# Kernel tuning notes

Hardware: AMD Instinct MI355X
Metric: run time of the kernel (lower is better)

The kernel has to match this reference:

```python
import jax, jax.numpy as jnp
import numpy as np

THRESH = 1.0   # kwargs_spikes['thresh']
VRESET = 0.0   # kwargs_spikes['vreset'] (not None -> hard reset branch)

@jax.custom_vjp
def rectangle_spike(x):
    # Rectangle surrogate-gradient spike fn: forward heaviside
    return (x >= 0.0).astype(x.dtype)

def _rs_fwd(x):
    return rectangle_spike(x), x

def _rs_bwd(x, g):
    # rectangular surrogate: grad passes where |u - thresh| < 0.5
    return (g * (jnp.abs(x) < 0.5).astype(g.dtype),)

rectangle_spike.defvjp(_rs_fwd, _rs_bwd)

def conv2d(x, w, b):
    # NCHW same-padding conv (padding = kernel_size // 2 with k=3 == SAME)
    y = jax.lax.conv_general_dilated(x, w, (1, 1), 'SAME',
                                     dimension_numbers=('NCHW', 'OIHW', 'NCHW'))
    return y + b[None, :, None, None]

def setup_inputs() -> dict:
    key = jax.random.key(0)
    ks = jax.random.split(key, 4)
    B, T, Cin, H, W = 8, 5, 64, 64, 64
    Cout, K = 64, 3
    # event-frame style sparse binary input
    events = (jax.random.uniform(ks[0], (B, T, Cin, H, W)) < 0.3).astype(jnp.float32)
    scale_in = 1.0 / np.sqrt(Cin * K * K)
    w_in = (jax.random.normal(ks[1], (2 * Cout, Cin, K, K)) * scale_in).astype(jnp.float32)
    b_in = jnp.zeros((2 * Cout,), jnp.float32)
    scale_g = 1.0 / np.sqrt(Cout * K * K)
    w_gate = (jax.random.normal(ks[2], (2 * Cout, Cout, K, K)) * scale_g).astype(jnp.float32)
    b_gate = jnp.zeros((2 * Cout,), jnp.float32)
    thresh_decay = jnp.ones((Cout,), jnp.float32) * 0.9
    return {'events': events, 'w_in': w_in, 'b_in': b_in,
            'w_gate': w_gate, 'b_gate': b_gate, 'thresh_decay': thresh_decay}

def reference(events, w_in, b_in, w_gate, b_gate, thresh_decay):
    # events: [B, T, Cin, H, W] -> [T, B, Cin, H, W], time-reversed (index_select with
    # descending indices, as in the torch forward)
    ev = jnp.flip(jnp.swapaxes(events, 0, 1), axis=0)
    T, B, _, H, W = ev.shape
    Cout = thresh_decay.shape[0]
    vmem0 = jnp.zeros((B, Cout, H, W), ev.dtype)
    spike0 = jnp.zeros((B, Cout, H, W), ev.dtype)

    def step(carry, xs):
        vmem, spike_last = carry
        x, t = xs
        # input path and recurrent gate path each emit 2*Cout channels:
        # first half = current injection, second half = gate pre-activation
        cur_in, gate_in = jnp.split(conv2d(x, w_in, b_in), 2, axis=1)
        cur_g, gate_g = jnp.split(conv2d(spike_last, w_gate, b_gate), 2, axis=1)
        gate = jax.nn.sigmoid(gate_in + gate_g)
        current = cur_in + cur_g
        # per-channel decaying threshold: thresh * thresh_decay^t
        thresh_t = THRESH * thresh_decay[None, :, None, None] ** t
        vmem = gate * vmem + current
        spike = rectangle_spike(vmem - thresh_t)
        # vreset is not None -> hard reset to VRESET where spiked
        vmem = vmem * (1.0 - spike) + VRESET * spike
        return (vmem, spike), spike

    _, spikes = jax.lax.scan(step, (vmem0, spike0),
                             (ev, jnp.arange(T, dtype=ev.dtype)))
    # readout='avg': average firing map over time steps  [B, Cout, H, W]
    return jnp.mean(spikes, axis=0)
```

## Files before the change

kernel.cpp:

```cpp
#include <hip/hip_runtime.h>
#include <cmath>


typedef __attribute__((ext_vector_type(4))) int intx4;

#define HW 64
#define TT 5
#define PLANE 4096
#define CSTR 144
#define USIZE (4 * 66 * CSTR)
#define WPL 147456

__global__ __launch_bounds__(256) void prep_w(
    const float* __restrict__ w_in, const float* __restrict__ w_gate,
    const float* __restrict__ b_in, const float* __restrict__ b_gate,
    const float* __restrict__ tdec,
    signed char* __restrict__ Wp, float* __restrict__ tabs)
{
  const int idx = blockIdx.x * 256 + threadIdx.x;
  if (idx < 9216) {
    const int o   = idx & 127;
    const int q   = (idx >> 7) & 3;
    const int ks  = (idx >> 9) & 1;
    const int tap = idx >> 10;
    const int g = o >> 4, i = o & 15;
    const int row = (i >> 3) * 64 + g * 8 + (i & 7);
    int p1[4], p2[4], p3[4], p4[4];
#pragma unroll
    for (int wd = 0; wd < 4; ++wd) {
      int v1 = 0, v2 = 0, v3 = 0, v4 = 0;
#pragma unroll
      for (int jb = 0; jb < 4; ++jb) {
        const int j = wd * 4 + jb;
        const int c = ks * 64 + q * 16 + j;
        const float w = (c < 64) ? w_in[(row * 64 + c) * 9 + tap]
                                 : w_gate[(row * 64 + (c - 64)) * 9 + tap];
        float a1 = fminf(fmaxf(rintf(w * 256.f), -127.f), 127.f);
        float r1 = w * 256.f - a1;
        float a2 = rintf(r1 * 128.f);
        float r2 = r1 * 128.f - a2;
        float a3 = rintf(r2 * 128.f);
        float r3 = r2 * 128.f - a3;
        float a4 = rintf(r3 * 128.f);
        v1 |= ((int)a1 & 255) << (8 * jb);
        v2 |= ((int)a2 & 255) << (8 * jb);
        v3 |= ((int)a3 & 255) << (8 * jb);
        v4 |= ((int)a4 & 255) << (8 * jb);
      }
      p1[wd] = v1; p2[wd] = v2; p3[wd] = v3; p4[wd] = v4;
    }
    intx4* d = (intx4*)(Wp + (size_t)idx * 16);
    d[0]                          = intx4{p1[0], p1[1], p1[2], p1[3]};
    *(intx4*)((char*)d + WPL)     = intx4{p2[0], p2[1], p2[2], p2[3]};
    *(intx4*)((char*)d + 2 * WPL) = intx4{p3[0], p3[1], p3[2], p3[3]};
    *(intx4*)((char*)d + 3 * WPL) = intx4{p4[0], p4[1], p4[2], p4[3]};
  }
  if (idx < 448) {
    if (idx < 128) tabs[idx] = b_in[idx] + b_gate[idx];
    else {
      const int t = (idx - 128) >> 6, co = (idx - 128) & 63;
      tabs[idx] = powf(tdec[co], (float)t);
    }
  }
}

__global__ __launch_bounds__(256) void prep_ev(
    const float* __restrict__ ev, signed char* __restrict__ evb)
{
  const int row  = blockIdx.x * 4 + (threadIdx.x >> 6);
  const int w    = threadIdx.x & 63;
  const int b  = row / (TT * HW);
  const int rm = row % (TT * HW);
  const int tp = rm / HW;
  const int h  = rm % HW;
  const float* src = ev + ((size_t)(b * TT + tp) * 64) * PLANE + h * HW + w;
  signed char* dst = evb + ((size_t)((b * TT + tp) * PLANE + h * HW + w)) * 64;
#pragma unroll
  for (int k = 0; k < 8; ++k) {
    unsigned long long pk = 0;
#pragma unroll
    for (int j = 0; j < 8; ++j)
      pk |= (src[(size_t)(k * 8 + j) * PLANE] != 0.f)
              ? (1ull << (8 * j)) : 0ull;
    *(unsigned long long*)(dst + k * 8) = pk;
  }
}

__global__ __launch_bounds__(1024, 4) void snn_step(
    const signed char* __restrict__ evb,
    const signed char* __restrict__ Wp,
    const float*       __restrict__ tabs,
    float*             __restrict__ vmem,
    const signed char* __restrict__ s_src,
    signed char*       __restrict__ s_dst,
    float*             __restrict__ outp,
    int t)
{
  __shared__ signed char U[USIZE];

  const int tid = threadIdx.x;
  const int b   = blockIdx.x >> 5;
  const int r0  = (blockIdx.x & 31) * 2;

  const int lane = tid & 63;
  const int g    = (tid >> 6) & 7;
  const int hf   = tid >> 9;
  const int ln   = lane & 15;
  const int q    = lane >> 4;

  for (int i = tid; i < USIZE / 16; i += 1024) ((intx4*)U)[i] = intx4{0, 0, 0, 0};

  const int srow = tid >> 8;
  const int scol = (tid >> 2) & 63;
  const int sch  = tid & 3;
  const int sr   = r0 + srow - 1;
  const bool svalid = (sr >= 0) && (sr < HW);
  signed char* du = U + (srow * 66 + scol + 1) * CSTR + sch * 32;
  const signed char* gsrc = nullptr;
  if (svalid) {
    gsrc = (sch < 2)
      ? evb + ((size_t)(b * TT + (TT - 1 - t)) * PLANE + sr * HW + scol) * 64 + sch * 32
      : s_src + ((size_t)((b * HW + sr) * HW + scol)) * 64 + (sch - 2) * 32;
  }
  __syncthreads();
  if (svalid) {
    *(intx4*)(du)      = *(const intx4*)(gsrc);
    *(intx4*)(du + 16) = *(const intx4*)(gsrc + 16);
  }
  __syncthreads();

  intx4 acc1[4], acc2[4], acc3[4], acc4[4];
#pragma unroll
  for (int tt = 0; tt < 4; ++tt) {
    acc1[tt] = intx4{0,0,0,0}; acc2[tt] = intx4{0,0,0,0};
    acc3[tt] = intx4{0,0,0,0}; acc4[tt] = intx4{0,0,0,0};
  }

  const int laneB = ln * CSTR + q * 16;
  const signed char* wlane = Wp + q * 2048 + (g * 16 + ln) * 16;

  for (int tap = 0; tap < 9; ++tap) {
    const int kh = (tap * 11) >> 5;
    const int kw = tap - 3 * kh;
#pragma unroll
    for (int ks = 0; ks < 2; ++ks) {
      const signed char* wp = wlane + (tap * 2 + ks) * 8192;
      const intx4 A1 = *(const intx4*)(wp);
      const intx4 A2 = *(const intx4*)(wp + WPL);
      const intx4 A3 = *(const intx4*)(wp + 2 * WPL);
      const intx4 A4 = *(const intx4*)(wp + 3 * WPL);
      const signed char* ub = U + (hf + kh) * (66 * CSTR) + kw * CSTR + ks * 64 + laneB;
#pragma unroll
      for (int tt = 0; tt < 4; ++tt) {
        const intx4 B = *(const intx4*)(ub + tt * (16 * CSTR));
        acc1[tt] = __builtin_amdgcn_mfma_i32_16x16x64_i8(A1, B, acc1[tt], 0, 0, 0);
        acc2[tt] = __builtin_amdgcn_mfma_i32_16x16x64_i8(A2, B, acc2[tt], 0, 0, 0);
        acc3[tt] = __builtin_amdgcn_mfma_i32_16x16x64_i8(A3, B, acc3[tt], 0, 0, 0);
        acc4[tt] = __builtin_amdgcn_mfma_i32_16x16x64_i8(A4, B, acc4[tt], 0, 0, 0);
      }
    }
  }

  const bool t0 = (t == 0), tL = (t == TT - 1);
  const int co0 = g * 8 + (q & 1) * 4;
  float bc[4], bg[4], th[4];
#pragma unroll
  for (int r = 0; r < 4; ++r) {
    bc[r] = tabs[co0 + r];
    bg[r] = tabs[64 + co0 + r];
    th[r] = tabs[128 + t * 64 + co0 + r];
  }
  const int hh = r0 + hf;
#pragma unroll
  for (int tt = 0; tt < 4; ++tt) {
    const int col = tt * 16 + ln;
    uint fm = 0;
#pragma unroll
    for (int r = 0; r < 4; ++r) {
      const float mine = fmaf((float)acc1[tt][r], 0x1p-8f,
                         fmaf((float)acc2[tt][r], 0x1p-15f,
                         fmaf((float)acc3[tt][r], 0x1p-22f,
                              (float)acc4[tt][r] * 0x1p-29f)));
      const float other = __shfl_xor(mine, 32, 64);
      if (q < 2) {
        const int co = co0 + r;
        const size_t idx = ((size_t)((b * 64 + co) * HW + hh)) * HW + col;
        const float cur  = mine + bc[r];
        const float gp   = other + bg[r];
        const float gate = 1.f / (1.f + expf(-gp));
        const float v    = gate * vmem[idx] + cur;
        const bool fired = (v >= th[r]);
        vmem[idx] = fired ? 0.f : v;
        fm |= fired ? (1u << (8 * r)) : 0u;
        float o = (t0 ? 0.f : outp[idx]) + (fired ? 1.f : 0.f);
        if (tL) o *= 0.2f;
        outp[idx] = o;
      }
    }
    if (q < 2)
      *(uint*)(s_dst + ((size_t)((b * HW + hh) * HW + col)) * 64 + co0) = fm;
  }
}

extern "C" void kernel_launch(void* const* d_in, const int* in_sizes, int n_in,
                              void* d_out, int out_size, void* d_ws, size_t ws_size,
                              hipStream_t stream) {
  const float* events = (const float*)d_in[0];
  const float* w_in   = (const float*)d_in[1];
  const float* b_in   = (const float*)d_in[2];
  const float* w_gate = (const float*)d_in[3];
  const float* b_gate = (const float*)d_in[4];
  const float* tdec   = (const float*)d_in[5];
  float* out = (float*)d_out;

  char* base = (char*)d_ws;
  float*       vmem = (float*)base;
  signed char* sA   = (signed char*)(base + 8388608);
  signed char* sB   = (signed char*)(base + 10485760);
  signed char* evb  = (signed char*)(base + 12582912);
  signed char* Wp   = (signed char*)(base + 23068672);
  float*       tabs = (float*)(base + 23658496);

  hipMemsetAsync(base, 0, 10485760, stream);

  hipLaunchKernelGGL(prep_w,  dim3(36),  dim3(256), 0, stream,
                     w_in, w_gate, b_in, b_gate, tdec, Wp, tabs);
  hipLaunchKernelGGL(prep_ev, dim3(640), dim3(256), 0, stream, events, evb);

  for (int t = 0; t < TT; ++t) {
    const signed char* ssrc = (t & 1) ? sB : sA;
    signed char*       sdst = (t & 1) ? sA : sB;
    hipLaunchKernelGGL(snn_step, dim3(256), dim3(1024), 0, stream,
                       evb, Wp, tabs, vmem, ssrc, sdst, out, t);
  }
}
```

Measured before the change: 247.3 us.

## Fuse event binarization into step kernel and drop memset and prep_ev

Removes the separate prep_ev kernel that packed float events into an int8 channel-last buffer; each step kernel now reads the float event planes directly, binarizes 16 channels per thread, and writes them into the shared-memory tile. The workspace memset is removed by treating vmem as zero and skipping the spike-state load at t==0. This saves one launch, a memset, and the round trip through the intermediate buffer. In exchange each step reads 4-byte floats with a channel-strided (PLANE) access pattern instead of compact int8 rows. The global loads are issued before the shared-memory zeroing to overlap their latency.

```diff
diff --git a/kernel.cpp b/kernel.cpp
--- a/kernel.cpp
+++ b/kernel.cpp
@@ -64,30 +64,8 @@
   }
 }
 
-__global__ __launch_bounds__(256) void prep_ev(
-    const float* __restrict__ ev, signed char* __restrict__ evb)
-{
-  const int row  = blockIdx.x * 4 + (threadIdx.x >> 6);
-  const int w    = threadIdx.x & 63;
-  const int b  = row / (TT * HW);
-  const int rm = row % (TT * HW);
-  const int tp = rm / HW;
-  const int h  = rm % HW;
-  const float* src = ev + ((size_t)(b * TT + tp) * 64) * PLANE + h * HW + w;
-  signed char* dst = evb + ((size_t)((b * TT + tp) * PLANE + h * HW + w)) * 64;
-#pragma unroll
-  for (int k = 0; k < 8; ++k) {
-    unsigned long long pk = 0;
-#pragma unroll
-    for (int j = 0; j < 8; ++j)
-      pk |= (src[(size_t)(k * 8 + j) * PLANE] != 0.f)
-              ? (1ull << (8 * j)) : 0ull;
-    *(unsigned long long*)(dst + k * 8) = pk;
-  }
-}
-
 __global__ __launch_bounds__(1024, 4) void snn_step(
-    const signed char* __restrict__ evb,
+    const float*       __restrict__ events,
     const signed char* __restrict__ Wp,
     const float*       __restrict__ tabs,
     float*             __restrict__ vmem,
@@ -108,24 +86,36 @@
   const int ln   = lane & 15;
   const int q    = lane >> 4;
 
-  for (int i = tid; i < USIZE / 16; i += 1024) ((intx4*)U)[i] = intx4{0, 0, 0, 0};
-
   const int srow = tid >> 8;
   const int scol = (tid >> 2) & 63;
   const int sch  = tid & 3;
   const int sr   = r0 + srow - 1;
   const bool svalid = (sr >= 0) && (sr < HW);
-  signed char* du = U + (srow * 66 + scol + 1) * CSTR + sch * 32;
-  const signed char* gsrc = nullptr;
+
+  float ef[16];
+  intx4 sv = intx4{0, 0, 0, 0};
   if (svalid) {
-    gsrc = (sch < 2)
-      ? evb + ((size_t)(b * TT + (TT - 1 - t)) * PLANE + sr * HW + scol) * 64 + sch * 32
-      : s_src + ((size_t)((b * HW + sr) * HW + scol)) * 64 + (sch - 2) * 32;
-  }
+    const float* es = events
+        + ((size_t)((b * TT + (TT - 1 - t)) * 64 + sch * 16)) * PLANE
+        + sr * HW + scol;
+#pragma unroll
+    for (int j = 0; j < 16; ++j) ef[j] = es[(size_t)j * PLANE];
+    if (t > 0)
+      sv = *(const intx4*)(s_src + ((size_t)((b * HW + sr) * HW + scol)) * 64
+                           + sch * 16);
+  }
+
+  for (int i = tid; i < USIZE / 16; i += 1024) ((intx4*)U)[i] = intx4{0, 0, 0, 0};
   __syncthreads();
+
   if (svalid) {
-    *(intx4*)(du)      = *(const intx4*)(gsrc);
-    *(intx4*)(du + 16) = *(const intx4*)(gsrc + 16);
+    uint dw[4] = {0u, 0u, 0u, 0u};
+#pragma unroll
+    for (int j = 0; j < 16; ++j)
+      dw[j >> 2] |= (ef[j] != 0.f ? 1u : 0u) << (8 * (j & 3));
+    signed char* du = U + (srow * 66 + scol + 1) * CSTR + sch * 16;
+    *(intx4*)du        = intx4{(int)dw[0], (int)dw[1], (int)dw[2], (int)dw[3]};
+    *(intx4*)(du + 64) = sv;
   }
   __syncthreads();
 
@@ -188,7 +178,8 @@
         const float cur  = mine + bc[r];
         const float gp   = other + bg[r];
         const float gate = 1.f / (1.f + expf(-gp));
-        const float v    = gate * vmem[idx] + cur;
+        const float vprev = t0 ? 0.f : vmem[idx];
+        const float v    = gate * vprev + cur;
         const bool fired = (v >= th[r]);
         vmem[idx] = fired ? 0.f : v;
         fm |= fired ? (1u << (8 * r)) : 0u;
@@ -217,20 +208,16 @@
   float*       vmem = (float*)base;
   signed char* sA   = (signed char*)(base + 8388608);
   signed char* sB   = (signed char*)(base + 10485760);
-  signed char* evb  = (signed char*)(base + 12582912);
-  signed char* Wp   = (signed char*)(base + 23068672);
-  float*       tabs = (float*)(base + 23658496);
-
-  hipMemsetAsync(base, 0, 10485760, stream);
-
-  hipLaunchKernelGGL(prep_w,  dim3(36),  dim3(256), 0, stream,
+  signed char* Wp   = (signed char*)(base + 12582912);
+  float*       tabs = (float*)(base + 13172736);
+
+  hipLaunchKernelGGL(prep_w, dim3(36), dim3(256), 0, stream,
                      w_in, w_gate, b_in, b_gate, tdec, Wp, tabs);
-  hipLaunchKernelGGL(prep_ev, dim3(640), dim3(256), 0, stream, events, evb);
 
   for (int t = 0; t < TT; ++t) {
     const signed char* ssrc = (t & 1) ? sB : sA;
     signed char*       sdst = (t & 1) ? sA : sB;
     hipLaunchKernelGGL(snn_step, dim3(256), dim3(1024), 0, stream,
-                       evb, Wp, tabs, vmem, ssrc, sdst, out, t);
+                       events, Wp, tabs, vmem, ssrc, sdst, out, t);
   }
 }
```

After: 236.5 us. 4.4% less time.

## Use channel-last vmem/count buffers, drop memset, and overlap staging loads

Applied to the files above, without the earlier changes.

Stores membrane potential and spike counts in pixel-major, channel-contiguous scratch buffers so each lane reads and writes four channels with one float4 access instead of strided scalar accesses. The final step writes the averaged output in NCHW layout directly. The workspace memset goes away: step 0 treats vmem and counts as zero and skips loading the recurrent spike input. Global staging loads are issued before the LDS zero-fill so their latency overlaps it. The cost is a larger workspace and a scattered write on the last step.

```diff
diff --git a/kernel.cpp b/kernel.cpp
--- a/kernel.cpp
+++ b/kernel.cpp
@@ -90,10 +90,11 @@
     const signed char* __restrict__ evb,
     const signed char* __restrict__ Wp,
     const float*       __restrict__ tabs,
-    float*             __restrict__ vmem,
+    float*             __restrict__ vmemC,
+    float*             __restrict__ outC,
     const signed char* __restrict__ s_src,
     signed char*       __restrict__ s_dst,
-    float*             __restrict__ outp,
+    float*             __restrict__ outF,
     int t)
 {
   __shared__ signed char U[USIZE];
@@ -108,24 +109,35 @@
   const int ln   = lane & 15;
   const int q    = lane >> 4;
 
-  for (int i = tid; i < USIZE / 16; i += 1024) ((intx4*)U)[i] = intx4{0, 0, 0, 0};
-
   const int srow = tid >> 8;
   const int scol = (tid >> 2) & 63;
   const int sch  = tid & 3;
   const int sr   = r0 + srow - 1;
   const bool svalid = (sr >= 0) && (sr < HW);
-  signed char* du = U + (srow * 66 + scol + 1) * CSTR + sch * 32;
-  const signed char* gsrc = nullptr;
+
+  intx4 st0 = intx4{0,0,0,0}, st1 = intx4{0,0,0,0};
+  bool sstore = false;
   if (svalid) {
-    gsrc = (sch < 2)
-      ? evb + ((size_t)(b * TT + (TT - 1 - t)) * PLANE + sr * HW + scol) * 64 + sch * 32
-      : s_src + ((size_t)((b * HW + sr) * HW + scol)) * 64 + (sch - 2) * 32;
-  }
+    if (sch < 2) {
+      const signed char* gs = evb
+          + ((size_t)((b * TT + (TT - 1 - t)) * PLANE + sr * HW + scol)) * 64
+          + sch * 32;
+      st0 = *(const intx4*)gs; st1 = *(const intx4*)(gs + 16);
+      sstore = true;
+    } else if (t > 0) {
+      const signed char* gs = s_src
+          + ((size_t)((b * HW + sr) * HW + scol)) * 64 + (sch - 2) * 32;
+      st0 = *(const intx4*)gs; st1 = *(const intx4*)(gs + 16);
+      sstore = true;
+    }
+  }
+
+  for (int i = tid; i < USIZE / 16; i += 1024) ((intx4*)U)[i] = intx4{0, 0, 0, 0};
   __syncthreads();
-  if (svalid) {
-    *(intx4*)(du)      = *(const intx4*)(gsrc);
-    *(intx4*)(du + 16) = *(const intx4*)(gsrc + 16);
+  if (sstore) {
+    signed char* du = U + (srow * 66 + scol + 1) * CSTR + sch * 32;
+    *(intx4*)du        = st0;
+    *(intx4*)(du + 16) = st1;
   }
   __syncthreads();
 
@@ -171,34 +183,47 @@
     th[r] = tabs[128 + t * 64 + co0 + r];
   }
   const int hh = r0 + hf;
+  const size_t pxbase = ((size_t)(b * HW + hh) * HW) * 64 + co0;
 #pragma unroll
   for (int tt = 0; tt < 4; ++tt) {
     const int col = tt * 16 + ln;
-    uint fm = 0;
-#pragma unroll
-    for (int r = 0; r < 4; ++r) {
-      const float mine = fmaf((float)acc1[tt][r], 0x1p-8f,
-                         fmaf((float)acc2[tt][r], 0x1p-15f,
-                         fmaf((float)acc3[tt][r], 0x1p-22f,
-                              (float)acc4[tt][r] * 0x1p-29f)));
-      const float other = __shfl_xor(mine, 32, 64);
-      if (q < 2) {
-        const int co = co0 + r;
-        const size_t idx = ((size_t)((b * 64 + co) * HW + hh)) * HW + col;
-        const float cur  = mine + bc[r];
-        const float gp   = other + bg[r];
+    const size_t o = pxbase + (size_t)col * 64;
+    float mine[4];
+#pragma unroll
+    for (int r = 0; r < 4; ++r)
+      mine[r] = fmaf((float)acc1[tt][r], 0x1p-8f,
+                fmaf((float)acc2[tt][r], 0x1p-15f,
+                fmaf((float)acc3[tt][r], 0x1p-22f,
+                     (float)acc4[tt][r] * 0x1p-29f)));
+    float other[4];
+#pragma unroll
+    for (int r = 0; r < 4; ++r) other[r] = __shfl_xor(mine[r], 32, 64);
+    if (q < 2) {
+      float4 vm4 = t0 ? float4{0.f,0.f,0.f,0.f} : *(const float4*)&vmemC[o];
+      float4 oc4 = t0 ? float4{0.f,0.f,0.f,0.f} : *(const float4*)&outC[o];
+      uint fm = 0;
+#pragma unroll
+      for (int r = 0; r < 4; ++r) {
+        const float cur  = mine[r] + bc[r];
+        const float gp   = other[r] + bg[r];
         const float gate = 1.f / (1.f + expf(-gp));
-        const float v    = gate * vmem[idx] + cur;
+        const float v    = gate * (&vm4.x)[r] + cur;
         const bool fired = (v >= th[r]);
-        vmem[idx] = fired ? 0.f : v;
+        (&vm4.x)[r] = fired ? 0.f : v;
+        (&oc4.x)[r] += fired ? 1.f : 0.f;
         fm |= fired ? (1u << (8 * r)) : 0u;
-        float o = (t0 ? 0.f : outp[idx]) + (fired ? 1.f : 0.f);
-        if (tL) o *= 0.2f;
-        outp[idx] = o;
-      }
-    }
-    if (q < 2)
-      *(uint*)(s_dst + ((size_t)((b * HW + hh) * HW + col)) * 64 + co0) = fm;
+      }
+      if (!tL) {
+        *(float4*)&vmemC[o] = vm4;
+        *(float4*)&outC[o]  = oc4;
+        *(uint*)&s_dst[o]   = fm;
+      } else {
+#pragma unroll
+        for (int r = 0; r < 4; ++r)
+          outF[((size_t)((b * 64 + co0 + r) * HW + hh)) * HW + col]
+              = (&oc4.x)[r] * 0.2f;
+      }
+    }
   }
 }
 
@@ -214,14 +239,13 @@
   float* out = (float*)d_out;
 
   char* base = (char*)d_ws;
-  float*       vmem = (float*)base;
-  signed char* sA   = (signed char*)(base + 8388608);
-  signed char* sB   = (signed char*)(base + 10485760);
-  signed char* evb  = (signed char*)(base + 12582912);
-  signed char* Wp   = (signed char*)(base + 23068672);
-  float*       tabs = (float*)(base + 23658496);
-
-  hipMemsetAsync(base, 0, 10485760, stream);
+  float*       vmemC = (float*)base;
+  float*       outC  = (float*)(base + 8388608);
+  signed char* sA    = (signed char*)(base + 16777216);
+  signed char* sB    = (signed char*)(base + 18874368);
+  signed char* evb   = (signed char*)(base + 20971520);
+  signed char* Wp    = (signed char*)(base + 31457280);
+  float*       tabs  = (float*)(base + 32047104);
 
   hipLaunchKernelGGL(prep_w,  dim3(36),  dim3(256), 0, stream,
                      w_in, w_gate, b_in, b_gate, tdec, Wp, tabs);
@@ -231,6 +255,6 @@
     const signed char* ssrc = (t & 1) ? sB : sA;
     signed char*       sdst = (t & 1) ? sA : sB;
     hipLaunchKernelGGL(snn_step, dim3(256), dim3(1024), 0, stream,
-                       evb, Wp, tabs, vmem, ssrc, sdst, out, t);
-  }
-}
+                       evb, Wp, tabs, vmemC, outC, ssrc, sdst, out, t);
+  }
+}
```

After: 234.2 us. -5.3%, faster.
